# Performance work log

Measured on AMD Instinct MI355X. Metric: run time of the kernel, lower is better.

## Reference

```python
import jax, jax.numpy as jnp
import numpy as np
from math import sqrt

DIM = 2048
NUM_HEADS = 16
HEAD_DIM = DIM // NUM_HEADS
BSZ, SEQ = 2, 2048


def setup_inputs() -> dict:
    key = jax.random.key(0)
    kx, kq, kk, kv, ko = jax.random.split(key, 5)
    x = jax.random.normal(kx, (BSZ, SEQ, DIM), dtype=jnp.float32)
    # causal additive mask, broadcastable to [B, H, S, S]
    neg = jnp.finfo(jnp.float32).min
    mask = jnp.where(jnp.tril(jnp.ones((SEQ, SEQ), dtype=bool)), 0.0, neg)[None, None]
    s = 1.0 / sqrt(DIM)
    Wq = jax.random.normal(kq, (DIM, DIM), dtype=jnp.float32) * s
    Wk = jax.random.normal(kk, (DIM, DIM), dtype=jnp.float32) * s
    Wv = jax.random.normal(kv, (DIM, DIM), dtype=jnp.float32) * s
    Wo = jax.random.normal(ko, (DIM, DIM), dtype=jnp.float32) * s
    return {"x": x, "mask": mask, "Wq": Wq, "Wk": Wk, "Wv": Wv, "Wo": Wo}


def reference(x, mask, Wq, Wk, Wv, Wo):
    b, s, _ = x.shape
    # nn.Linear: y = x @ W.T
    def proj(W):
        return (x @ W.T).reshape(b, s, NUM_HEADS, HEAD_DIM).transpose(0, 2, 1, 3)  # [b,h,s,d]
    q, k, v = proj(Wq), proj(Wk), proj(Wv)
    scores = jnp.einsum('bhqd,bhkd->bhqk', q, k) / sqrt(HEAD_DIM)
    scores = scores + mask
    attn = jax.nn.softmax(scores.astype(jnp.float32), axis=-1).astype(q.dtype)
    out = jnp.einsum('bhqk,bhkd->bhqd', attn, v)
    out = out.transpose(0, 2, 1, 3).reshape(b, s, -1)
    return out @ Wo.T
```

## Files before the change

kernel.cpp:

```cpp
#include <hip/hip_runtime.h>
#include <hip/hip_bf16.h>
#include <stdint.h>

#define DIM 2048
#define NHEADS 16
#define HDIM 128
#define BATCH 2
#define SEQLEN 2048

using bf16x8 = __attribute__((ext_vector_type(8))) __bf16;
using f32x4  = __attribute__((ext_vector_type(4))) float;
typedef unsigned short u16;
typedef unsigned int u32;

__device__ __forceinline__ void cp16(const void* g, void* lds) {
  __builtin_amdgcn_global_load_lds((const __attribute__((address_space(1))) u32*)g,
                                   (__attribute__((address_space(3))) u32*)lds, 16, 0, 0);
}

__device__ __forceinline__ u16 f2b(float f) {
  u32 u = __float_as_uint(f);
  return (u16)((u + 0x7fffu + ((u >> 16) & 1u)) >> 16);
}

__global__ __launch_bounds__(256) void cvt_kernel(
    const float* __restrict__ x,
    const float* __restrict__ Wq, const float* __restrict__ Wk,
    const float* __restrict__ Wv, const float* __restrict__ Wo,
    u16* __restrict__ xb, u16* __restrict__ wqb, u16* __restrict__ wkb,
    u16* __restrict__ wvb, u16* __restrict__ wob)
{
  const size_t Wsz = (size_t)DIM * DIM;
  const float* src; u16* dst;
  switch (blockIdx.y) {
    case 0:  src = x;        dst = xb;        break;
    case 1:  src = x + Wsz;  dst = xb + Wsz;  break;
    case 2:  src = Wq;       dst = wqb;       break;
    case 3:  src = Wk;       dst = wkb;       break;
    case 4:  src = Wv;       dst = wvb;       break;
    default: src = Wo;       dst = wob;       break;
  }
  size_t i = ((size_t)blockIdx.x * 256 + threadIdx.x) * 8;
  float4 a = *(const float4*)(src + i);
  float4 b = *(const float4*)(src + i + 4);
  union { bf16x8 v; u16 s[8]; } u;
  u.s[0] = f2b(a.x); u.s[1] = f2b(a.y); u.s[2] = f2b(a.z); u.s[3] = f2b(a.w);
  u.s[4] = f2b(b.x); u.s[5] = f2b(b.y); u.s[6] = f2b(b.z); u.s[7] = f2b(b.w);
  *(bf16x8*)(dst + i) = u.v;
}

template<int OM>
__device__ __forceinline__ void gemm_body(const u16* __restrict__ A, const u16* __restrict__ B,
                                          void* Cp, u16* As, u16* Bs)
{
  const int tid = threadIdx.x;
  const int w = tid >> 6, l = tid & 63;
  const int wm = w >> 1, wn = w & 1;
  const int quad = l >> 4, ln = l & 15;
  const int bm = blockIdx.y, bn = blockIdx.x;

  f32x4 acc[4][4];
#pragma unroll
  for (int i = 0; i < 4; ++i)
#pragma unroll
    for (int jx = 0; jx < 4; ++jx) acc[i][jx] = (f32x4){0.f, 0.f, 0.f, 0.f};

  const u16* Ag = A + (size_t)(bm * 128 + (tid >> 2)) * DIM + (tid & 3) * 8;
  const u16* Bg = B + (size_t)(bn * 128 + (tid >> 2)) * DIM + (tid & 3) * 8;
  u16* AsW = As + w * 512;
  u16* BsW = Bs + w * 512;

  for (int k0 = 0; k0 < DIM; k0 += 32) {
    cp16(Ag + k0, AsW);
    cp16(Ag + k0 + 64 * DIM, AsW + 2048);
    cp16(Bg + k0, BsW);
    cp16(Bg + k0 + 64 * DIM, BsW + 2048);
    __syncthreads();

    bf16x8 af[4], bfr[4];
#pragma unroll
    for (int mi = 0; mi < 4; ++mi)
      af[mi] = *(const bf16x8*)(As + (wm * 64 + mi * 16 + ln) * 32 + quad * 8);
#pragma unroll
    for (int ni = 0; ni < 4; ++ni)
      bfr[ni] = *(const bf16x8*)(Bs + (wn * 64 + ni * 16 + ln) * 32 + quad * 8);
#pragma unroll
    for (int mi = 0; mi < 4; ++mi)
#pragma unroll
      for (int ni = 0; ni < 4; ++ni)
        acc[mi][ni] = __builtin_amdgcn_mfma_f32_16x16x32_bf16(af[mi], bfr[ni], acc[mi][ni], 0, 0, 0);
    __syncthreads();
  }

  if constexpr (OM == 2) {
#pragma unroll
    for (int mi = 0; mi < 4; ++mi)
#pragma unroll
      for (int ni = 0; ni < 4; ++ni) {
        int i0 = bm * 128 + wm * 64 + mi * 16 + quad * 4;
        int jj = bn * 128 + wn * 64 + ni * 16 + ln;
        int b = i0 >> 11, s0 = i0 & 2047, hh = jj >> 7, d = jj & 127;
        ushort4 v4;
        v4.x = f2b(acc[mi][ni][0]); v4.y = f2b(acc[mi][ni][1]);
        v4.z = f2b(acc[mi][ni][2]); v4.w = f2b(acc[mi][ni][3]);
        size_t off = ((size_t)((b * NHEADS + hh) * HDIM + d)) * SEQLEN + s0;
        *(ushort4*)((u16*)Cp + off) = v4;
      }
  } else {
#pragma unroll
    for (int mi = 0; mi < 4; ++mi)
#pragma unroll
      for (int ni = 0; ni < 4; ++ni)
#pragma unroll
        for (int r = 0; r < 4; ++r) {
          int i = bm * 128 + wm * 64 + mi * 16 + quad * 4 + r;
          int jj = bn * 128 + wn * 64 + ni * 16 + ln;
          if constexpr (OM == 1) {
            int b = i >> 11, s = i & 2047, hh = jj >> 7, d = jj & 127;
            size_t off = ((size_t)((b * NHEADS + hh) * SEQLEN + s)) * HDIM + d;
            ((u16*)Cp)[off] = f2b(acc[mi][ni][r]);
          } else {
            ((float*)Cp)[(size_t)i * DIM + jj] = acc[mi][ni][r];
          }
        }
  }
}

__global__ __launch_bounds__(256) void qkv_kernel(const u16* __restrict__ xb,
    const u16* __restrict__ Wq, const u16* __restrict__ Wk, const u16* __restrict__ Wv,
    u16* __restrict__ Q, u16* __restrict__ Kk, u16* __restrict__ V)
{
  __shared__ __align__(16) u16 As[128 * 32];
  __shared__ __align__(16) u16 Bs[128 * 32];
  if (blockIdx.z == 0)      gemm_body<1>(xb, Wq, Q, As, Bs);
  else if (blockIdx.z == 1) gemm_body<1>(xb, Wk, Kk, As, Bs);
  else                      gemm_body<2>(xb, Wv, V, As, Bs);
}

__global__ __launch_bounds__(256) void out_kernel(const u16* __restrict__ ctx,
    const u16* __restrict__ Wo, float* __restrict__ out)
{
  __shared__ __align__(16) u16 As[128 * 32];
  __shared__ __align__(16) u16 Bs[128 * 32];
  gemm_body<0>(ctx, Wo, out, As, Bs);
}

__global__ __launch_bounds__(256, 2) void attn_kernel(const u16* __restrict__ Q,
    const u16* __restrict__ K, const u16* __restrict__ VT, u16* __restrict__ ctx)
{
  __shared__ __align__(16) u16 Ks[2][64 * 128];
  __shared__ __align__(16) u16 Vt[2][128 * 64];
  __shared__ __align__(16) u16 Ps[4][32 * 64];

  const int tid = threadIdx.x;
  const int w = tid >> 6, l = tid & 63;
  const int quad = l >> 4, ln = l & 15;

  const int j = blockIdx.x;
  const int b = j >> 8;
  const int kk = j & 255;
  const int h = kk >> 4;
  const int q0 = kk & 15;
  const int qt = b ? (15 - q0) : q0;

  const size_t head_off = (size_t)(b * NHEADS + h) * SEQLEN * HDIM;
  const u16* Qg = Q + head_off + (size_t)qt * 128 * HDIM;
  const u16* Kh = K + head_off;
  const u16* Vh = VT + head_off;

  const int swsrc = (tid * 8) ^ (((tid >> 4) & 7) << 3);
  const int swr = (ln & 7) << 3;

  const int vrow = w * 8 + (l >> 3);
  const int vcol = (((l & 7) ^ (l >> 3)) << 3);

  union { bf16x8 v; u16 s[8]; } bo;
#pragma unroll
  for (int e = 0; e < 8; ++e) bo.s[e] = (ln == 0) ? (u16)0x3F80 : (u16)0;
  const bf16x8 bones = bo.v;

  bf16x8 aq[2][4];
#pragma unroll
  for (int chunk = 0; chunk < 2; ++chunk) {
    u16* base = Ks[0] + w * 512;
    const u16* g = Qg + chunk * 8192 + swsrc;
    cp16(g, base); cp16(g + 2048, base + 2048);
    cp16(g + 4096, base + 4096); cp16(g + 6144, base + 6144);
    __syncthreads();
    if ((w >> 1) == chunk) {
      int rl = (w & 1) * 32;
#pragma unroll
      for (int mi = 0; mi < 2; ++mi)
#pragma unroll
        for (int kb = 0; kb < 4; ++kb)
          aq[mi][kb] = *(const bf16x8*)(Ks[0] + (((rl + mi * 16 + ln) * 128 + kb * 32 + quad * 8) ^ swr));
    }
    __syncthreads();
  }

  float m_run[2][4];
  f32x4 o[2][8];
  f32x4 ol[2];
#pragma unroll
  for (int mi = 0; mi < 2; ++mi) {
#pragma unroll
    for (int r = 0; r < 4; ++r) m_run[mi][r] = -1e30f;
#pragma unroll
    for (int cb = 0; cb < 8; ++cb) o[mi][cb] = (f32x4){0.f, 0.f, 0.f, 0.f};
    ol[mi] = (f32x4){0.f, 0.f, 0.f, 0.f};
  }

  const float c2 = 0.08838834764831845f * 1.4426950408889634f;
  const int NT = 2 * qt + 2;

  {
    u16* kb_ = Ks[0] + w * 512;
    const u16* kg = Kh + swsrc;
    cp16(kg, kb_); cp16(kg + 2048, kb_ + 2048);
    cp16(kg + 4096, kb_ + 4096); cp16(kg + 6144, kb_ + 6144);
    u16* vb_ = Vt[0] + w * 512;
    const u16* vg = Vh + (size_t)vrow * SEQLEN + vcol;
    cp16(vg, vb_); cp16(vg + 32 * SEQLEN, vb_ + 2048);
    cp16(vg + 64 * SEQLEN, vb_ + 4096); cp16(vg + 96 * SEQLEN, vb_ + 6144);
  }

  int cur = 0;
  for (int ct = 0; ct < NT; ++ct) {
    if (ct + 1 < NT) {
      u16* kb_ = Ks[cur ^ 1] + w * 512;
      const u16* kg = Kh + (size_t)(ct + 1) * 64 * HDIM + swsrc;
      cp16(kg, kb_); cp16(kg + 2048, kb_ + 2048);
      cp16(kg + 4096, kb_ + 4096); cp16(kg + 6144, kb_ + 6144);
      u16* vb_ = Vt[cur ^ 1] + w * 512;
      const u16* vg = Vh + (size_t)vrow * SEQLEN + (ct + 1) * 64 + vcol;
      cp16(vg, vb_); cp16(vg + 32 * SEQLEN, vb_ + 2048);
      cp16(vg + 64 * SEQLEN, vb_ + 4096); cp16(vg + 96 * SEQLEN, vb_ + 6144);
      asm volatile("s_waitcnt vmcnt(8)" ::: "memory");
    } else {
      asm volatile("s_waitcnt vmcnt(0)" ::: "memory");
    }
    __builtin_amdgcn_s_barrier();
    __builtin_amdgcn_sched_barrier(0);

    const u16* KsC = Ks[cur];
    const u16* VtC = Vt[cur];
    const bool active = !(ct == NT - 1 && w < 2);

    if (active) {
      f32x4 sc[2][4];
#pragma unroll
      for (int mi = 0; mi < 2; ++mi)
#pragma unroll
        for (int nb = 0; nb < 4; ++nb) sc[mi][nb] = (f32x4){0.f, 0.f, 0.f, 0.f};
      __builtin_amdgcn_s_setprio(1);
#pragma unroll
      for (int kb = 0; kb < 4; ++kb) {
        bf16x8 bk[4];
#pragma unroll
        for (int nb = 0; nb < 4; ++nb)
          bk[nb] = *(const bf16x8*)(KsC + (((nb * 16 + ln) * 128 + kb * 32 + quad * 8) ^ swr));
#pragma unroll
        for (int mi = 0; mi < 2; ++mi)
#pragma unroll
          for (int nb = 0; nb < 4; ++nb)
            sc[mi][nb] = __builtin_amdgcn_mfma_f32_16x16x32_bf16(aq[mi][kb], bk[nb], sc[mi][nb], 0, 0, 0);
      }
      __builtin_amdgcn_s_setprio(0);

      if (ct >= 2 * qt) {
        int dd = (2 * qt - ct) * 64;
#pragma unroll
        for (int mi = 0; mi < 2; ++mi)
#pragma unroll
          for (int nb = 0; nb < 4; ++nb) {
            int col = nb * 16 + ln;
#pragma unroll
            for (int r = 0; r < 4; ++r) {
              int row = w * 32 + mi * 16 + quad * 4 + r;
              if (col > row + dd) sc[mi][nb][r] = -1e30f;
            }
          }
      }

      float mxv[2][4];
      bool grow = false;
#pragma unroll
      for (int mi = 0; mi < 2; ++mi)
#pragma unroll
        for (int r = 0; r < 4; ++r) {
          float mx = fmaxf(fmaxf(sc[mi][0][r], sc[mi][1][r]), fmaxf(sc[mi][2][r], sc[mi][3][r]));
#pragma unroll
          for (int s = 1; s < 16; s <<= 1) mx = fmaxf(mx, __shfl_xor(mx, s, 64));
          mxv[mi][r] = mx;
          grow = grow || (mx > m_run[mi][r]);
        }

      if (__any(grow)) {
#pragma unroll
        for (int mi = 0; mi < 2; ++mi)
#pragma unroll
          for (int r = 0; r < 4; ++r) {
            float mnew = fmaxf(m_run[mi][r], mxv[mi][r]);
            float alpha = exp2f((m_run[mi][r] - mnew) * c2);
            m_run[mi][r] = mnew;
#pragma unroll
            for (int cb = 0; cb < 8; ++cb) o[mi][cb][r] *= alpha;
            ol[mi][r] *= alpha;
          }
      }

#pragma unroll
      for (int mi = 0; mi < 2; ++mi)
#pragma unroll
        for (int r = 0; r < 4; ++r) {
          int row = mi * 16 + quad * 4 + r;
#pragma unroll
          for (int nb = 0; nb < 4; ++nb)
            Ps[w][(row * 64 + nb * 16 + ln) ^ ((row & 7) << 3)] =
                f2b(exp2f((sc[mi][nb][r] - m_run[mi][r]) * c2));
        }

      __builtin_amdgcn_sched_barrier(0);
      asm volatile("s_waitcnt lgkmcnt(0)" ::: "memory");
      __builtin_amdgcn_sched_barrier(0);

#pragma unroll
      for (int tb = 0; tb < 2; ++tb) {
        bf16x8 ap[2];
#pragma unroll
        for (int mi = 0; mi < 2; ++mi)
          ap[mi] = *(const bf16x8*)(&Ps[w][0] + (((mi * 16 + ln) * 64 + tb * 32 + quad * 8) ^ swr));
        __builtin_amdgcn_s_setprio(1);
#pragma unroll
        for (int cb = 0; cb < 8; ++cb) {
          bf16x8 bv = *(const bf16x8*)(VtC + ((cb * 16 + ln) * 64 + ((tb * 32 + quad * 8) ^ swr)));
#pragma unroll
          for (int mi = 0; mi < 2; ++mi)
            o[mi][cb] = __builtin_amdgcn_mfma_f32_16x16x32_bf16(ap[mi], bv, o[mi][cb], 0, 0, 0);
        }
#pragma unroll
        for (int mi = 0; mi < 2; ++mi)
          ol[mi] = __builtin_amdgcn_mfma_f32_16x16x32_bf16(ap[mi], bones, ol[mi], 0, 0, 0);
        __builtin_amdgcn_s_setprio(0);
      }
    }

    __builtin_amdgcn_sched_barrier(0);
    asm volatile("s_waitcnt lgkmcnt(0)" ::: "memory");
    __builtin_amdgcn_s_barrier();
    cur ^= 1;
  }

  float lv[2][4];
#pragma unroll
  for (int mi = 0; mi < 2; ++mi)
#pragma unroll
    for (int r = 0; r < 4; ++r)
      lv[mi][r] = __shfl(ol[mi][r], quad * 16, 64);

#pragma unroll
  for (int mi = 0; mi < 2; ++mi)
#pragma unroll
    for (int cb = 0; cb < 8; ++cb)
#pragma unroll
      for (int r = 0; r < 4; ++r) {
        float v = o[mi][cb][r] / lv[mi][r];
        int srow = qt * 128 + w * 32 + mi * 16 + quad * 4 + r;
        size_t off = ((size_t)(b * SEQLEN + srow)) * DIM + h * HDIM + cb * 16 + ln;
        ctx[off] = f2b(v);
      }
}

extern "C" void kernel_launch(void* const* d_in, const int* in_sizes, int n_in,
                              void* d_out, int out_size, void* d_ws, size_t ws_size,
                              hipStream_t stream) {
  const float* x  = (const float*)d_in[0];
  const float* Wq = (const float*)d_in[2];
  const float* Wk = (const float*)d_in[3];
  const float* Wv = (const float*)d_in[4];
  const float* Wo = (const float*)d_in[5];
  float* out = (float*)d_out;

  const size_t HSZ = (size_t)BATCH * NHEADS * SEQLEN * HDIM;
  const size_t WSZ = (size_t)DIM * DIM;
  u16* Qw  = (u16*)d_out;
  u16* xb  = Qw + HSZ;
  u16* wqb = (u16*)d_ws;
  u16* wkb = wqb + WSZ;
  u16* wvb = wkb + WSZ;
  u16* wob = wvb + WSZ;
  u16* Kw  = wob + WSZ;
  u16* Vw  = Kw + HSZ;
  u16* Cw  = Vw + HSZ;

  cvt_kernel<<<dim3(WSZ / (256 * 8), 6), 256, 0, stream>>>(
      x, Wq, Wk, Wv, Wo, xb, wqb, wkb, wvb, wob);
  qkv_kernel<<<dim3(DIM / 128, (BATCH * SEQLEN) / 128, 3), 256, 0, stream>>>(
      xb, wqb, wkb, wvb, Qw, Kw, Vw);
  attn_kernel<<<dim3(BATCH * NHEADS * (SEQLEN / 128)), 256, 0, stream>>>(Qw, Kw, Vw, Cw);
  out_kernel<<<dim3(DIM / 128, (BATCH * SEQLEN) / 128, 1), 256, 0, stream>>>(Cw, wob, out);
}
```

Before: 430.4 us.

## Split attention work across eight waves with 16 query rows each

The attention kernel moves from 4 waves handling 32 query rows each to 512 threads (8 waves) handling 16 rows each. Cooperative K/V tile loads are split across twice as many threads, so each thread issues half the copies and the waitcnt drops to match. Per-wave register use for accumulators falls, which allows more waves per CU to hide latency. In exchange, each K/V fragment read from LDS feeds fewer MFMAs, which raises LDS read traffic per unit of compute.

Measured after the change: 454.2 us. 5.5% more time.

```diff
diff --git a/kernel.cpp b/kernel.cpp
--- a/kernel.cpp
+++ b/kernel.cpp
@@ -145,12 +145,12 @@
   gemm_body<0>(ctx, Wo, out, As, Bs);
 }
 
-__global__ __launch_bounds__(256, 2) void attn_kernel(const u16* __restrict__ Q,
+__global__ __launch_bounds__(512, 2) void attn_kernel(const u16* __restrict__ Q,
     const u16* __restrict__ K, const u16* __restrict__ VT, u16* __restrict__ ctx)
 {
   __shared__ __align__(16) u16 Ks[2][64 * 128];
   __shared__ __align__(16) u16 Vt[2][128 * 64];
-  __shared__ __align__(16) u16 Ps[4][32 * 64];
+  __shared__ __align__(16) u16 Ps[8][16 * 64];
 
   const int tid = threadIdx.x;
   const int w = tid >> 6, l = tid & 63;
@@ -179,36 +179,30 @@
   for (int e = 0; e < 8; ++e) bo.s[e] = (ln == 0) ? (u16)0x3F80 : (u16)0;
   const bf16x8 bones = bo.v;
 
-  bf16x8 aq[2][4];
+  bf16x8 aq[4];
 #pragma unroll
   for (int chunk = 0; chunk < 2; ++chunk) {
     u16* base = Ks[0] + w * 512;
     const u16* g = Qg + chunk * 8192 + swsrc;
-    cp16(g, base); cp16(g + 2048, base + 2048);
-    cp16(g + 4096, base + 4096); cp16(g + 6144, base + 6144);
+    cp16(g, base); cp16(g + 4096, base + 4096);
     __syncthreads();
-    if ((w >> 1) == chunk) {
-      int rl = (w & 1) * 32;
-#pragma unroll
-      for (int mi = 0; mi < 2; ++mi)
-#pragma unroll
-        for (int kb = 0; kb < 4; ++kb)
-          aq[mi][kb] = *(const bf16x8*)(Ks[0] + (((rl + mi * 16 + ln) * 128 + kb * 32 + quad * 8) ^ swr));
+    if ((w >> 2) == chunk) {
+      int rl = (w & 3) * 16;
+#pragma unroll
+      for (int kb = 0; kb < 4; ++kb)
+        aq[kb] = *(const bf16x8*)(Ks[0] + (((rl + ln) * 128 + kb * 32 + quad * 8) ^ swr));
     }
     __syncthreads();
   }
 
-  float m_run[2][4];
-  f32x4 o[2][8];
-  f32x4 ol[2];
-#pragma unroll
-  for (int mi = 0; mi < 2; ++mi) {
-#pragma unroll
-    for (int r = 0; r < 4; ++r) m_run[mi][r] = -1e30f;
-#pragma unroll
-    for (int cb = 0; cb < 8; ++cb) o[mi][cb] = (f32x4){0.f, 0.f, 0.f, 0.f};
-    ol[mi] = (f32x4){0.f, 0.f, 0.f, 0.f};
-  }
+  float m_run[4];
+  f32x4 o[8];
+  f32x4 ol;
+#pragma unroll
+  for (int r = 0; r < 4; ++r) m_run[r] = -1e30f;
+#pragma unroll
+  for (int cb = 0; cb < 8; ++cb) o[cb] = (f32x4){0.f, 0.f, 0.f, 0.f};
+  ol = (f32x4){0.f, 0.f, 0.f, 0.f};
 
   const float c2 = 0.08838834764831845f * 1.4426950408889634f;
   const int NT = 2 * qt + 2;
@@ -216,12 +210,10 @@
   {
     u16* kb_ = Ks[0] + w * 512;
     const u16* kg = Kh + swsrc;
-    cp16(kg, kb_); cp16(kg + 2048, kb_ + 2048);
-    cp16(kg + 4096, kb_ + 4096); cp16(kg + 6144, kb_ + 6144);
+    cp16(kg, kb_); cp16(kg + 4096, kb_ + 4096);
     u16* vb_ = Vt[0] + w * 512;
     const u16* vg = Vh + (size_t)vrow * SEQLEN + vcol;
-    cp16(vg, vb_); cp16(vg + 32 * SEQLEN, vb_ + 2048);
-    cp16(vg + 64 * SEQLEN, vb_ + 4096); cp16(vg + 96 * SEQLEN, vb_ + 6144);
+    cp16(vg, vb_); cp16(vg + 64 * SEQLEN, vb_ + 4096);
   }
 
   int cur = 0;
@@ -229,13 +221,11 @@
     if (ct + 1 < NT) {
       u16* kb_ = Ks[cur ^ 1] + w * 512;
       const u16* kg = Kh + (size_t)(ct + 1) * 64 * HDIM + swsrc;
-      cp16(kg, kb_); cp16(kg + 2048, kb_ + 2048);
-      cp16(kg + 4096, kb_ + 4096); cp16(kg + 6144, kb_ + 6144);
+      cp16(kg, kb_); cp16(kg + 4096, kb_ + 4096);
       u16* vb_ = Vt[cur ^ 1] + w * 512;
       const u16* vg = Vh + (size_t)vrow * SEQLEN + (ct + 1) * 64 + vcol;
-      cp16(vg, vb_); cp16(vg + 32 * SEQLEN, vb_ + 2048);
-      cp16(vg + 64 * SEQLEN, vb_ + 4096); cp16(vg + 96 * SEQLEN, vb_ + 6144);
-      asm volatile("s_waitcnt vmcnt(8)" ::: "memory");
+      cp16(vg, vb_); cp16(vg + 64 * SEQLEN, vb_ + 4096);
+      asm volatile("s_waitcnt vmcnt(4)" ::: "memory");
     } else {
       asm volatile("s_waitcnt vmcnt(0)" ::: "memory");
     }
@@ -244,14 +234,12 @@
 
     const u16* KsC = Ks[cur];
     const u16* VtC = Vt[cur];
-    const bool active = !(ct == NT - 1 && w < 2);
+    const bool active = !(ct == NT - 1 && w < 4);
 
     if (active) {
-      f32x4 sc[2][4];
-#pragma unroll
-      for (int mi = 0; mi < 2; ++mi)
-#pragma unroll
-        for (int nb = 0; nb < 4; ++nb) sc[mi][nb] = (f32x4){0.f, 0.f, 0.f, 0.f};
+      f32x4 sc[4];
+#pragma unroll
+      for (int nb = 0; nb < 4; ++nb) sc[nb] = (f32x4){0.f, 0.f, 0.f, 0.f};
       __builtin_amdgcn_s_setprio(1);
 #pragma unroll
       for (int kb = 0; kb < 4; ++kb) {
@@ -260,65 +248,55 @@
         for (int nb = 0; nb < 4; ++nb)
           bk[nb] = *(const bf16x8*)(KsC + (((nb * 16 + ln) * 128 + kb * 32 + quad * 8) ^ swr));
 #pragma unroll
-        for (int mi = 0; mi < 2; ++mi)
-#pragma unroll
-          for (int nb = 0; nb < 4; ++nb)
-            sc[mi][nb] = __builtin_amdgcn_mfma_f32_16x16x32_bf16(aq[mi][kb], bk[nb], sc[mi][nb], 0, 0, 0);
+        for (int nb = 0; nb < 4; ++nb)
+          sc[nb] = __builtin_amdgcn_mfma_f32_16x16x32_bf16(aq[kb], bk[nb], sc[nb], 0, 0, 0);
       }
       __builtin_amdgcn_s_setprio(0);
 
       if (ct >= 2 * qt) {
         int dd = (2 * qt - ct) * 64;
 #pragma unroll
-        for (int mi = 0; mi < 2; ++mi)
-#pragma unroll
-          for (int nb = 0; nb < 4; ++nb) {
-            int col = nb * 16 + ln;
-#pragma unroll
-            for (int r = 0; r < 4; ++r) {
-              int row = w * 32 + mi * 16 + quad * 4 + r;
-              if (col > row + dd) sc[mi][nb][r] = -1e30f;
-            }
+        for (int nb = 0; nb < 4; ++nb) {
+          int col = nb * 16 + ln;
+#pragma unroll
+          for (int r = 0; r < 4; ++r) {
+            int row = w * 16 + quad * 4 + r;
+            if (col > row + dd) sc[nb][r] = -1e30f;
           }
-      }
-
-      float mxv[2][4];
+        }
+      }
+
+      float mxv[4];
       bool grow = false;
 #pragma unroll
-      for (int mi = 0; mi < 2; ++mi)
+      for (int r = 0; r < 4; ++r) {
+        float mx = fmaxf(fmaxf(sc[0][r], sc[1][r]), fmaxf(sc[2][r], sc[3][r]));
+#pragma unroll
+        for (int s = 1; s < 16; s <<= 1) mx = fmaxf(mx, __shfl_xor(mx, s, 64));
+        mxv[r] = mx;
+        grow = grow || (mx > m_run[r]);
+      }
+
+      if (__any(grow)) {
 #pragma unroll
         for (int r = 0; r < 4; ++r) {
-          float mx = fmaxf(fmaxf(sc[mi][0][r], sc[mi][1][r]), fmaxf(sc[mi][2][r], sc[mi][3][r]));
-#pragma unroll
-          for (int s = 1; s < 16; s <<= 1) mx = fmaxf(mx, __shfl_xor(mx, s, 64));
-          mxv[mi][r] = mx;
-          grow = grow || (mx > m_run[mi][r]);
+          float mnew = fmaxf(m_run[r], mxv[r]);
+          float alpha = exp2f((m_run[r] - mnew) * c2);
+          m_run[r] = mnew;
+#pragma unroll
+          for (int cb = 0; cb < 8; ++cb) o[cb][r] *= alpha;
+          ol[r] *= alpha;
         }
-
-      if (__any(grow)) {
-#pragma unroll
-        for (int mi = 0; mi < 2; ++mi)
-#pragma unroll
-          for (int r = 0; r < 4; ++r) {
-            float mnew = fmaxf(m_run[mi][r], mxv[mi][r]);
-            float alpha = exp2f((m_run[mi][r] - mnew) * c2);
-            m_run[mi][r] = mnew;
-#pragma unroll
-            for (int cb = 0; cb < 8; ++cb) o[mi][cb][r] *= alpha;
-            ol[mi][r] *= alpha;
-          }
-      }
-
-#pragma unroll
-      for (int mi = 0; mi < 2; ++mi)
-#pragma unroll
-        for (int r = 0; r < 4; ++r) {
-          int row = mi * 16 + quad * 4 + r;
-#pragma unroll
-          for (int nb = 0; nb < 4; ++nb)
-            Ps[w][(row * 64 + nb * 16 + ln) ^ ((row & 7) << 3)] =
-                f2b(exp2f((sc[mi][nb][r] - m_run[mi][r]) * c2));
-        }
+      }
+
+#pragma unroll
+      for (int r = 0; r < 4; ++r) {
+        int row = quad * 4 + r;
+#pragma unroll
+        for (int nb = 0; nb < 4; ++nb)
+          Ps[w][(row * 64 + nb * 16 + ln) ^ ((row & 7) << 3)] =
+              f2b(exp2f((sc[nb][r] - m_run[r]) * c2));
+      }
 
       __builtin_amdgcn_sched_barrier(0);
       asm volatile("s_waitcnt lgkmcnt(0)" ::: "memory");
@@ -326,21 +304,14 @@
 
 #pragma unroll
       for (int tb = 0; tb < 2; ++tb) {
-        bf16x8 ap[2];
-#pragma unroll
-        for (int mi = 0; mi < 2; ++mi)
-          ap[mi] = *(const bf16x8*)(&Ps[w][0] + (((mi * 16 + ln) * 64 + tb * 32 + quad * 8) ^ swr));
+        bf16x8 ap = *(const bf16x8*)(&Ps[w][0] + ((ln * 64 + tb * 32 + quad * 8) ^ swr));
         __builtin_amdgcn_s_setprio(1);
 #pragma unroll
         for (int cb = 0; cb < 8; ++cb) {
           bf16x8 bv = *(const bf16x8*)(VtC + ((cb * 16 + ln) * 64 + ((tb * 32 + quad * 8) ^ swr)));
-#pragma unroll
-          for (int mi = 0; mi < 2; ++mi)
-            o[mi][cb] = __builtin_amdgcn_mfma_f32_16x16x32_bf16(ap[mi], bv, o[mi][cb], 0, 0, 0);
+          o[cb] = __builtin_amdgcn_mfma_f32_16x16x32_bf16(ap, bv, o[cb], 0, 0, 0);
         }
-#pragma unroll
-        for (int mi = 0; mi < 2; ++mi)
-          ol[mi] = __builtin_amdgcn_mfma_f32_16x16x32_bf16(ap[mi], bones, ol[mi], 0, 0, 0);
+        ol = __builtin_amdgcn_mfma_f32_16x16x32_bf16(ap, bones, ol, 0, 0, 0);
         __builtin_amdgcn_s_setprio(0);
       }
     }
@@ -351,24 +322,20 @@
     cur ^= 1;
   }
 
-  float lv[2][4];
-#pragma unroll
-  for (int mi = 0; mi < 2; ++mi)
-#pragma unroll
-    for (int r = 0; r < 4; ++r)
-      lv[mi][r] = __shfl(ol[mi][r], quad * 16, 64);
-
-#pragma unroll
-  for (int mi = 0; mi < 2; ++mi)
-#pragma unroll
-    for (int cb = 0; cb < 8; ++cb)
-#pragma unroll
-      for (int r = 0; r < 4; ++r) {
-        float v = o[mi][cb][r] / lv[mi][r];
-        int srow = qt * 128 + w * 32 + mi * 16 + quad * 4 + r;
-        size_t off = ((size_t)(b * SEQLEN + srow)) * DIM + h * HDIM + cb * 16 + ln;
-        ctx[off] = f2b(v);
-      }
+  float lv[4];
+#pragma unroll
+  for (int r = 0; r < 4; ++r)
+    lv[r] = __shfl(ol[r], quad * 16, 64);
+
+#pragma unroll
+  for (int cb = 0; cb < 8; ++cb)
+#pragma unroll
+    for (int r = 0; r < 4; ++r) {
+      float v = o[cb][r] / lv[r];
+      int srow = qt * 128 + w * 16 + quad * 4 + r;
+      size_t off = ((size_t)(b * SEQLEN + srow)) * DIM + h * HDIM + cb * 16 + ln;
+      ctx[off] = f2b(v);
+    }
 }
 
 extern "C" void kernel_launch(void* const* d_in, const int* in_sizes, int n_in,
@@ -397,6 +364,6 @@
       x, Wq, Wk, Wv, Wo, xb, wqb, wkb, wvb, wob);
   qkv_kernel<<<dim3(DIM / 128, (BATCH * SEQLEN) / 128, 3), 256, 0, stream>>>(
       xb, wqb, wkb, wvb, Qw, Kw, Vw);
-  attn_kernel<<<dim3(BATCH * NHEADS * (SEQLEN / 128)), 256, 0, stream>>>(Qw, Kw, Vw, Cw);
+  attn_kernel<<<dim3(BATCH * NHEADS * (SEQLEN / 128)), 512, 0, stream>>>(Qw, Kw, Vw, Cw);
   out_kernel<<<dim3(DIM / 128, (BATCH * SEQLEN) / 128, 1), 256, 0, stream>>>(Cw, wob, out);
 }
```
